# Kernel tuning notes

Hardware: AMD Instinct MI355X
Metric: run time of the kernel (lower is better)

Reference implementation:

```python
import jax, jax.numpy as jnp
import numpy as np

D_MODEL = 1024
N_HEADS = 16
D_K = D_MODEL // N_HEADS


def setup_inputs() -> dict:
    key = jax.random.key(0)
    ks = jax.random.split(key, 9)
    s = 1.0 / np.sqrt(D_MODEL)
    x = jax.random.normal(ks[0], (4, 2048, D_MODEL), dtype=jnp.float32)
    def lin(kw, kb):
        W = jax.random.uniform(kw, (D_MODEL, D_MODEL), jnp.float32, -s, s)
        b = jax.random.uniform(kb, (D_MODEL,), jnp.float32, -s, s)
        return W, b
    w_q, b_q = lin(ks[1], ks[2])
    w_k, b_k = lin(ks[3], ks[4])
    w_v, b_v = lin(ks[5], ks[6])
    w_o, b_o = lin(ks[7], ks[8])
    return {"x": x, "w_q": w_q, "b_q": b_q, "w_k": w_k, "b_k": b_k,
            "w_v": w_v, "b_v": b_v, "w_o": w_o, "b_o": b_o}


def reference(x, w_q, b_q, w_k, b_k, w_v, b_v, w_o, b_o):
    B, S, _ = x.shape
    # projections; nn.Linear computes x @ W^T + b, here W stored as [in, out]
    def proj(W, b):
        return (x @ W + b).reshape(B, S, N_HEADS, D_K).transpose(0, 2, 1, 3)  # [B,H,S,Dk]
    q = proj(w_q, b_q)
    k = proj(w_k, b_k)
    v = proj(w_v, b_v)
    scores = jnp.einsum("bhsd,bhtd->bhst", q, k) / jnp.sqrt(jnp.float32(D_K))
    attn = jax.nn.softmax(scores, axis=-1)  # dropout p=0 -> identity
    ctx = jnp.einsum("bhst,bhtd->bhsd", attn, v)
    ctx = ctx.transpose(0, 2, 1, 3).reshape(B, S, D_MODEL)
    return ctx @ w_o + b_o
```

## Files before the change

kernel.cpp:

```cpp
#include <hip/hip_runtime.h>
#include <stdint.h>

typedef __attribute__((ext_vector_type(8))) short bf8;
typedef __attribute__((ext_vector_type(4))) float f4;
typedef __attribute__((ext_vector_type(16))) float f16v;
typedef __attribute__((ext_vector_type(4))) int i4;
typedef __attribute__((ext_vector_type(2))) int i2;
typedef unsigned short u16;

#define GLOAD16(gptr, lptr)                                                        \
    __builtin_amdgcn_global_load_lds((const __attribute__((address_space(1))) void*)(gptr), \
                                     (__attribute__((address_space(3))) void*)(lptr), 16, 0, 0)

static __device__ inline u16 f2bfbits(float f) {
    unsigned u = __float_as_uint(f);
    unsigned r = 0x7FFFu + ((u >> 16) & 1u);
    return (u16)((u + r) >> 16);
}

static __device__ inline int cvtpk(float lo, float hi) {
    int r;
    asm("v_cvt_pk_bf16_f32 %0, %1, %2" : "=v"(r) : "v"(lo), "v"(hi));
    return r;
}

__global__ void cvt_bf16(const float* __restrict__ in, u16* __restrict__ out, int n) {
    int i = (blockIdx.x * 256 + threadIdx.x) * 4;
    if (i < n) {
        float4 v = *(const float4*)(in + i);
        ushort4 o;
        o.x = f2bfbits(v.x); o.y = f2bfbits(v.y);
        o.z = f2bfbits(v.z); o.w = f2bfbits(v.w);
        *(ushort4*)(out + i) = o;
    }
}

__global__ void transpose4(const float* __restrict__ w0, const float* __restrict__ w1,
                           const float* __restrict__ w2, const float* __restrict__ w3,
                           u16* __restrict__ o0, u16* __restrict__ o1,
                           u16* __restrict__ o2, u16* __restrict__ o3) {
    __shared__ float tile[32][33];
    const float* w = blockIdx.z == 0 ? w0 : blockIdx.z == 1 ? w1 : blockIdx.z == 2 ? w2 : w3;
    u16* o = blockIdx.z == 0 ? o0 : blockIdx.z == 1 ? o1 : blockIdx.z == 2 ? o2 : o3;
    int bx = blockIdx.x * 32, by = blockIdx.y * 32;
    int tx = threadIdx.x, ty = threadIdx.y;
#pragma unroll
    for (int r = 0; r < 32; r += 8)
        tile[ty + r][tx] = w[(size_t)(by + ty + r) * 1024 + bx + tx];
    __syncthreads();
#pragma unroll
    for (int r = 0; r < 32; r += 8)
        o[(size_t)(bx + ty + r) * 1024 + by + tx] = f2bfbits(tile[tx][ty + r]);
}

static __device__ __attribute__((always_inline)) void gemm_pipe(
    const u16* __restrict__ A_, const u16* __restrict__ B_, int m0, int n0,
    char* Asl, char* Bsl, f4 (&acc)[4][4]) {
    const int tid = threadIdx.x;
    const int lane = tid & 63;
    const int l15 = lane & 15, lg = lane >> 4;
    const int wave = tid >> 6;
    const int wm = (wave >> 1) * 64, wn = (wave & 1) * 64;
    const int sr = lane >> 2, sc = lane & 3;

    const int rA0 = wave * 32 + sr;
    const int rA1 = rA0 + 16;
    const int cA0 = sc ^ ((rA0 >> 1) & 3);
    const int cA1 = sc ^ ((rA1 >> 1) & 3);
    const u16* pA0 = A_ + (size_t)(m0 + rA0) * 1024 + cA0 * 8;
    const u16* pA1 = A_ + (size_t)(m0 + rA1) * 1024 + cA1 * 8;
    const u16* pB0 = B_ + (size_t)(n0 + rA0) * 1024 + cA0 * 8;
    const u16* pB1 = B_ + (size_t)(n0 + rA1) * 1024 + cA1 * 8;

#pragma unroll
    for (int p = 0; p < 3; ++p) {
        const int k0 = p * 32;
        GLOAD16(pA0 + k0, Asl + p * 8192 + wave * 2048);
        GLOAD16(pA1 + k0, Asl + p * 8192 + wave * 2048 + 1024);
        GLOAD16(pB0 + k0, Bsl + p * 8192 + wave * 2048);
        GLOAD16(pB1 + k0, Bsl + p * 8192 + wave * 2048 + 1024);
    }

    int offA[4], offB[4];
#pragma unroll
    for (int i = 0; i < 4; ++i) {
        int r = wm + i * 16 + l15;
        offA[i] = r * 64 + ((lg ^ ((r >> 1) & 3)) * 16);
    }
#pragma unroll
    for (int j = 0; j < 4; ++j) {
        int r = wn + j * 16 + l15;
        offB[j] = r * 64 + ((lg ^ ((r >> 1) & 3)) * 16);
    }

    int b = 0;
    for (int kt = 0; kt < 32; ++kt) {
        asm volatile("s_waitcnt vmcnt(8)" ::: "memory");
        __builtin_amdgcn_s_barrier();
        __builtin_amdgcn_sched_barrier(0);
        const char* Ab = Asl + b * 8192;
        const char* Bb = Bsl + b * 8192;
        bf8 af[4], bfr[4];
#pragma unroll
        for (int i = 0; i < 4; ++i) af[i] = *(const bf8*)(Ab + offA[i]);
#pragma unroll
        for (int j = 0; j < 4; ++j) bfr[j] = *(const bf8*)(Bb + offB[j]);
        asm volatile("s_waitcnt lgkmcnt(0)" ::: "memory");
        __builtin_amdgcn_sched_barrier(0);
        __builtin_amdgcn_s_setprio(1);
#pragma unroll
        for (int i = 0; i < 4; ++i)
#pragma unroll
            for (int j = 0; j < 4; ++j)
                acc[i][j] = __builtin_amdgcn_mfma_f32_16x16x32_bf16(af[i], bfr[j], acc[i][j], 0, 0, 0);
        __builtin_amdgcn_s_setprio(0);
        __builtin_amdgcn_sched_barrier(0);
        __builtin_amdgcn_s_barrier();
        __builtin_amdgcn_sched_barrier(0);
        {
            const int k0 = ((kt + 3) & 31) * 32;
            GLOAD16(pA0 + k0, Asl + b * 8192 + wave * 2048);
            GLOAD16(pA1 + k0, Asl + b * 8192 + wave * 2048 + 1024);
            GLOAD16(pB0 + k0, Bsl + b * 8192 + wave * 2048);
            GLOAD16(pB1 + k0, Bsl + b * 8192 + wave * 2048 + 1024);
        }
        b = (b == 2) ? 0 : b + 1;
    }
    asm volatile("s_waitcnt vmcnt(0)" ::: "memory");
}

__global__ __launch_bounds__(256, 3) void gemm_qkv(
    const u16* __restrict__ A, const u16* __restrict__ BT,
    const float* __restrict__ bq, const float* __restrict__ bk, const float* __restrict__ bv,
    u16* __restrict__ qo, u16* __restrict__ ko, u16* __restrict__ vo) {
    __shared__ __align__(16) char Asl[24576];
    __shared__ __align__(16) char Bsl[24576];
    const int m0 = blockIdx.x * 128, n0 = blockIdx.y * 128;
    f4 acc[4][4] = {};
    gemm_pipe(A, BT, m0, n0, Asl, Bsl, acc);

    const int lane = threadIdx.x & 63;
    const int l15 = lane & 15, lg = lane >> 4;
    const int wave = threadIdx.x >> 6;
    const int wm = (wave >> 1) * 64, wn = (wave & 1) * 64;

    const int reg = n0 >> 10;
    const float* bp = reg == 0 ? bq : reg == 1 ? bk : bv;
    const float scq = reg == 0 ? 0.125f * 1.44269504088896340736f : 1.0f;
    float bj[4];
#pragma unroll
    for (int j = 0; j < 4; ++j) bj[j] = bp[(n0 + wn + j * 16 + l15) & 1023];

    if (reg < 2) {
        u16* outb = reg == 0 ? qo : ko;
#pragma unroll
        for (int i = 0; i < 4; ++i) {
            int gm = m0 + wm + i * 16 + lg * 4;
#pragma unroll
            for (int j = 0; j < 4; ++j) {
                int gn = (n0 + wn + j * 16 + l15) & 1023;
                int h = gn >> 6, d = gn & 63;
#pragma unroll
                for (int r = 0; r < 4; ++r) {
                    int m = gm + r;
                    int b_ = m >> 11, s = m & 2047;
                    float vv = (acc[i][j][r] + bj[j]) * scq;
                    outb[(((size_t)(b_ * 16 + h) * 2048) + s) * 64 + d] = f2bfbits(vv);
                }
            }
        }
    } else {
#pragma unroll
        for (int i = 0; i < 4; ++i) {
            int gm = m0 + wm + i * 16 + lg * 4;
            int b_ = gm >> 11, s0 = gm & 2047;
#pragma unroll
            for (int j = 0; j < 4; ++j) {
                int gn = (n0 + wn + j * 16 + l15) & 1023;
                int h = gn >> 6, d = gn & 63;
                ushort4 w;
                w.x = f2bfbits(acc[i][j][0] + bj[j]);
                w.y = f2bfbits(acc[i][j][1] + bj[j]);
                w.z = f2bfbits(acc[i][j][2] + bj[j]);
                w.w = f2bfbits(acc[i][j][3] + bj[j]);
                *(ushort4*)(vo + ((size_t)(b_ * 16 + h) * 64 + d) * 2048 + s0) = w;
            }
        }
    }
}

__global__ __launch_bounds__(256, 3) void gemm_o(
    const u16* __restrict__ A, const u16* __restrict__ BT,
    const float* __restrict__ bias, float* __restrict__ outf) {
    __shared__ __align__(16) char Asl[24576];
    __shared__ __align__(16) char Bsl[24576];
    const int m0 = blockIdx.x * 128, n0 = blockIdx.y * 128;
    f4 acc[4][4] = {};
    gemm_pipe(A, BT, m0, n0, Asl, Bsl, acc);

    const int lane = threadIdx.x & 63;
    const int l15 = lane & 15, lg = lane >> 4;
    const int wave = threadIdx.x >> 6;
    const int wm = (wave >> 1) * 64, wn = (wave & 1) * 64;

    float bj[4];
#pragma unroll
    for (int j = 0; j < 4; ++j) bj[j] = bias[n0 + wn + j * 16 + l15];
#pragma unroll
    for (int i = 0; i < 4; ++i) {
        int gm = m0 + wm + i * 16 + lg * 4;
#pragma unroll
        for (int j = 0; j < 4; ++j) {
            int gn = n0 + wn + j * 16 + l15;
#pragma unroll
            for (int r = 0; r < 4; ++r)
                outf[(size_t)(gm + r) * 1024 + gn] = acc[i][j][r] + bj[j];
        }
    }
}

static __device__ inline void softmax_pv(f16v s, float& l,
                                         f16v& ocA, f16v& ocB, const bf8* vf) {
    float s0 = 0.f, s1 = 0.f, s2 = 0.f, s3 = 0.f;
#pragma unroll
    for (int r = 0; r < 16; r += 4) {
        s[r + 0] = __builtin_amdgcn_exp2f(s[r + 0]); s0 += s[r + 0];
        s[r + 1] = __builtin_amdgcn_exp2f(s[r + 1]); s1 += s[r + 1];
        s[r + 2] = __builtin_amdgcn_exp2f(s[r + 2]); s2 += s[r + 2];
        s[r + 3] = __builtin_amdgcn_exp2f(s[r + 3]); s3 += s[r + 3];
    }
    float ps = (s0 + s1) + (s2 + s3);
    {
        i2 sw = __builtin_amdgcn_permlane32_swap(__float_as_int(ps), __float_as_int(ps), false, false);
        ps = __int_as_float(sw[0]) + __int_as_float(sw[1]);
    }
    l += ps;

    i4 w0, w1;
    {
        i2 r0 = __builtin_amdgcn_permlane32_swap(cvtpk(s[0], s[1]),   cvtpk(s[4], s[5]),   false, false);
        i2 r1 = __builtin_amdgcn_permlane32_swap(cvtpk(s[2], s[3]),   cvtpk(s[6], s[7]),   false, false);
        i2 r2 = __builtin_amdgcn_permlane32_swap(cvtpk(s[8], s[9]),   cvtpk(s[12], s[13]), false, false);
        i2 r3 = __builtin_amdgcn_permlane32_swap(cvtpk(s[10], s[11]), cvtpk(s[14], s[15]), false, false);
        w0[0] = r0[0]; w0[1] = r1[0]; w0[2] = r0[1]; w0[3] = r1[1];
        w1[0] = r2[0]; w1[1] = r3[0]; w1[2] = r2[1]; w1[3] = r3[1];
    }
    union { i4 i; bf8 h; } pa0, pa1;
    pa0.i = w0; pa1.i = w1;

    __builtin_amdgcn_s_setprio(1);
    ocA = __builtin_amdgcn_mfma_f32_32x32x16_bf16(vf[0], pa0.h, ocA, 0, 0, 0);
    ocB = __builtin_amdgcn_mfma_f32_32x32x16_bf16(vf[2], pa0.h, ocB, 0, 0, 0);
    ocA = __builtin_amdgcn_mfma_f32_32x32x16_bf16(vf[1], pa1.h, ocA, 0, 0, 0);
    ocB = __builtin_amdgcn_mfma_f32_32x32x16_bf16(vf[3], pa1.h, ocB, 0, 0, 0);
    __builtin_amdgcn_s_setprio(0);
}

__global__ __launch_bounds__(256, 4) void attn(
    const u16* __restrict__ Q, const u16* __restrict__ K, const u16* __restrict__ VT,
    u16* __restrict__ ctx) {
    __shared__ __align__(16) char Kl[2][8192];
    __shared__ __align__(16) char Vl[2][8192];

    const int tid = threadIdx.x;
    const int lane = tid & 63, wave = tid >> 6;
    const int l31 = lane & 31, hi = lane >> 5;

    const int g = blockIdx.x;
    const int xcd = g & 7, li = g >> 3;
    const int bh = xcd * 8 + (li >> 4);
    const int qblk = li & 15;
    const int q0 = qblk * 128 + wave * 32;

    const char* Kg = (const char*)(K + (size_t)bh * 2048 * 64);
    const char* Vg = (const char*)(VT + (size_t)bh * 64 * 2048);

    const int p0 = wave * 1024 + lane * 16;
    const int p1 = p0 + 4096;
    const int r0 = p0 >> 7, r1 = p1 >> 7;
    const int sc0 = (p0 & 127) ^ ((r0 & 7) << 4);
    const int sc1 = (p1 & 127) ^ ((r1 & 7) << 4);

    GLOAD16(Kg + (size_t)r0 * 128 + sc0, &Kl[0][wave * 1024]);
    GLOAD16(Kg + (size_t)r1 * 128 + sc1, &Kl[0][4096 + wave * 1024]);
    GLOAD16(Vg + (size_t)r0 * 4096 + sc0, &Vl[0][wave * 1024]);
    GLOAD16(Vg + (size_t)r1 * 4096 + sc1, &Vl[0][4096 + wave * 1024]);

    bf8 qf[4];
    {
        const u16* Qr = Q + ((size_t)bh * 2048 + q0 + l31) * 64 + hi * 8;
#pragma unroll
        for (int c = 0; c < 4; ++c) qf[c] = *(const bf8*)(Qr + c * 16);
    }

    f16v oc0 = {}, oc1 = {};
    float l = 0.f;
    const int sw = (l31 & 7) << 4;

    __syncthreads();

    int cur = 0;
    for (int it = 0; it < 32; ++it) {
        const int t0 = it * 64;
        if (it + 1 < 32) {
            const int nxt = cur ^ 1;
            const size_t tn = (size_t)(t0 + 64);
            GLOAD16(Kg + (tn + r0) * 128 + sc0, &Kl[nxt][wave * 1024]);
            GLOAD16(Kg + (tn + r1) * 128 + sc1, &Kl[nxt][4096 + wave * 1024]);
            GLOAD16(Vg + (size_t)r0 * 4096 + tn * 2 + sc0, &Vl[nxt][wave * 1024]);
            GLOAD16(Vg + (size_t)r1 * 4096 + tn * 2 + sc1, &Vl[nxt][4096 + wave * 1024]);
        }
        const char* Kb = Kl[cur];
        const char* Vb = Vl[cur];

#pragma unroll
        for (int st = 0; st < 2; ++st) {
            bf8 kf[4];
#pragma unroll
            for (int c = 0; c < 4; ++c)
                kf[c] = *(const bf8*)(Kb + (st * 32 + l31) * 128 + ((c * 32 + hi * 16) ^ sw));

            f16v s;
#pragma unroll
            for (int r = 0; r < 16; ++r) s[r] = -10.f;
            __builtin_amdgcn_s_setprio(1);
#pragma unroll
            for (int c = 0; c < 4; ++c)
                s = __builtin_amdgcn_mfma_f32_32x32x16_bf16(kf[c], qf[c], s, 0, 0, 0);
            __builtin_amdgcn_s_setprio(0);

            bf8 vf[4];
#pragma unroll
            for (int dt = 0; dt < 2; ++dt)
#pragma unroll
                for (int tc = 0; tc < 2; ++tc)
                    vf[dt * 2 + tc] = *(const bf8*)(Vb + (dt * 32 + l31) * 128 +
                                                    ((st * 64 + tc * 32 + hi * 16) ^ sw));

            softmax_pv(s, l, oc0, oc1, vf);
        }
        __syncthreads();
        cur ^= 1;
    }

    const int b_ = bh >> 4, hd = bh & 15;
    const float rl = __builtin_amdgcn_rcpf(l);
    u16* Cr = ctx + ((size_t)(b_ * 2048) + q0 + l31) * 1024 + hd * 64;
#pragma unroll
    for (int gi = 0; gi < 4; ++gi) {
        ushort4 w;
        w.x = f2bfbits(oc0[gi * 4 + 0] * rl);
        w.y = f2bfbits(oc0[gi * 4 + 1] * rl);
        w.z = f2bfbits(oc0[gi * 4 + 2] * rl);
        w.w = f2bfbits(oc0[gi * 4 + 3] * rl);
        *(ushort4*)(Cr + gi * 8 + hi * 4) = w;
    }
#pragma unroll
    for (int gi = 0; gi < 4; ++gi) {
        ushort4 w;
        w.x = f2bfbits(oc1[gi * 4 + 0] * rl);
        w.y = f2bfbits(oc1[gi * 4 + 1] * rl);
        w.z = f2bfbits(oc1[gi * 4 + 2] * rl);
        w.w = f2bfbits(oc1[gi * 4 + 3] * rl);
        *(ushort4*)(Cr + 32 + gi * 8 + hi * 4) = w;
    }
}

extern "C" void kernel_launch(void* const* d_in, const int* in_sizes, int n_in,
                              void* d_out, int out_size, void* d_ws, size_t ws_size,
                              hipStream_t stream) {
    const float* x  = (const float*)d_in[0];
    const float* wq = (const float*)d_in[1];
    const float* bq = (const float*)d_in[2];
    const float* wk = (const float*)d_in[3];
    const float* bk = (const float*)d_in[4];
    const float* wv = (const float*)d_in[5];
    const float* bv = (const float*)d_in[6];
    const float* wo = (const float*)d_in[7];
    const float* bo = (const float*)d_in[8];
    float* out = (float*)d_out;

    char* ws = (char*)d_ws;
    u16* xb  = (u16*)ws;
    u16* wtq = (u16*)(ws + (size_t)(16 << 20));
    u16* wtk = wtq + 1024 * 1024;
    u16* wtv = wtk + 1024 * 1024;
    u16* wto = wtv + 1024 * 1024;
    u16* q   = (u16*)(ws + (size_t)(24 << 20));
    u16* k   = q + 8192 * 1024;
    u16* vt  = k + 8192 * 1024;
    u16* ctx = vt + 8192 * 1024;

    hipLaunchKernelGGL(cvt_bf16, dim3(8192), dim3(256), 0, stream, x, xb, 8192 * 1024);
    hipLaunchKernelGGL(transpose4, dim3(32, 32, 4), dim3(32, 8), 0, stream,
                       wq, wk, wv, wo, wtq, wtk, wtv, wto);
    hipLaunchKernelGGL(gemm_qkv, dim3(64, 24), dim3(256), 0, stream,
                       xb, wtq, bq, bk, bv, q, k, vt);
    hipLaunchKernelGGL(attn, dim3(1024), dim3(256), 0, stream, q, k, vt, ctx);
    hipLaunchKernelGGL(gemm_o, dim3(64, 8), dim3(256), 0, stream, ctx, wto, bo, out);
}
```

Baseline: 189.7 us.

## Prefetch K/V tiles two iterations ahead with partial vmcnt waits

Restructures the attention loop's double-buffered K/V pipeline. Both buffers are prefetched before the loop, and each iteration waits only on the older loads via s_waitcnt vmcnt(4) plus a raw barrier. After compute, the freed buffer is refilled with the tile two steps ahead. This replaces the full __syncthreads drain each iteration so global loads stay in flight longer. The last iterations issue redundant wrapped loads, which adds some extra memory traffic.

```diff
diff --git a/kernel.cpp b/kernel.cpp
--- a/kernel.cpp
+++ b/kernel.cpp
@@ -281,11 +281,6 @@
     const int sc0 = (p0 & 127) ^ ((r0 & 7) << 4);
     const int sc1 = (p1 & 127) ^ ((r1 & 7) << 4);
 
-    GLOAD16(Kg + (size_t)r0 * 128 + sc0, &Kl[0][wave * 1024]);
-    GLOAD16(Kg + (size_t)r1 * 128 + sc1, &Kl[0][4096 + wave * 1024]);
-    GLOAD16(Vg + (size_t)r0 * 4096 + sc0, &Vl[0][wave * 1024]);
-    GLOAD16(Vg + (size_t)r1 * 4096 + sc1, &Vl[0][4096 + wave * 1024]);
-
     bf8 qf[4];
     {
         const u16* Qr = Q + ((size_t)bh * 2048 + q0 + l31) * 64 + hi * 8;
@@ -293,23 +288,23 @@
         for (int c = 0; c < 4; ++c) qf[c] = *(const bf8*)(Qr + c * 16);
     }
 
+#pragma unroll
+    for (int p = 0; p < 2; ++p) {
+        GLOAD16(Kg + (size_t)(p * 64 + r0) * 128 + sc0, &Kl[p][wave * 1024]);
+        GLOAD16(Kg + (size_t)(p * 64 + r1) * 128 + sc1, &Kl[p][4096 + wave * 1024]);
+        GLOAD16(Vg + (size_t)r0 * 4096 + p * 128 + sc0, &Vl[p][wave * 1024]);
+        GLOAD16(Vg + (size_t)r1 * 4096 + p * 128 + sc1, &Vl[p][4096 + wave * 1024]);
+    }
+
     f16v oc0 = {}, oc1 = {};
     float l = 0.f;
     const int sw = (l31 & 7) << 4;
 
-    __syncthreads();
-
-    int cur = 0;
     for (int it = 0; it < 32; ++it) {
-        const int t0 = it * 64;
-        if (it + 1 < 32) {
-            const int nxt = cur ^ 1;
-            const size_t tn = (size_t)(t0 + 64);
-            GLOAD16(Kg + (tn + r0) * 128 + sc0, &Kl[nxt][wave * 1024]);
-            GLOAD16(Kg + (tn + r1) * 128 + sc1, &Kl[nxt][4096 + wave * 1024]);
-            GLOAD16(Vg + (size_t)r0 * 4096 + tn * 2 + sc0, &Vl[nxt][wave * 1024]);
-            GLOAD16(Vg + (size_t)r1 * 4096 + tn * 2 + sc1, &Vl[nxt][4096 + wave * 1024]);
-        }
+        const int cur = it & 1;
+        asm volatile("s_waitcnt vmcnt(4)" ::: "memory");
+        __builtin_amdgcn_s_barrier();
+        __builtin_amdgcn_sched_barrier(0);
         const char* Kb = Kl[cur];
         const char* Vb = Vl[cur];
 
@@ -339,8 +334,16 @@
 
             softmax_pv(s, l, oc0, oc1, vf);
         }
-        __syncthreads();
-        cur ^= 1;
+        __builtin_amdgcn_sched_barrier(0);
+        __builtin_amdgcn_s_barrier();
+        __builtin_amdgcn_sched_barrier(0);
+        {
+            const int tt = (it + 2) & 31;
+            GLOAD16(Kg + (size_t)(tt * 64 + r0) * 128 + sc0, &Kl[cur][wave * 1024]);
+            GLOAD16(Kg + (size_t)(tt * 64 + r1) * 128 + sc1, &Kl[cur][4096 + wave * 1024]);
+            GLOAD16(Vg + (size_t)r0 * 4096 + tt * 128 + sc0, &Vl[cur][wave * 1024]);
+            GLOAD16(Vg + (size_t)r1 * 4096 + tt * 128 + sc1, &Vl[cur][4096 + wave * 1024]);
+        }
     }
 
     const int b_ = bh >> 4, hd = bh & 15;
```

New measurement: 190.2 us. No clear change (+0.3%).
